# Optimization experiments

Hardware: AMD Instinct MI355X
Metric: run time of the kernel (lower is better)

Reference implementation:

```python
import jax, jax.numpy as jnp
import numpy as np

N_QUBITS = 24          # must be divisible by 3
DIM = 2 ** N_QUBITS    # 16777216 amplitudes
N_GROUPS = N_QUBITS // 3  # 8 disjoint 3-qubit gate applications


def setup_inputs() -> dict:
    key = jax.random.key(0)
    k1, k2, k3 = jax.random.split(key, 3)
    feature = jax.random.normal(k1, (DIM,), dtype=jnp.float32)
    # Build a random 8x8 unitary as expm of an anti-Hermitian generator,
    # mirroring equivar_gate_matrix = expm(generator) in the original.
    m = (jax.random.normal(k2, (8, 8), dtype=jnp.float32)
         + 1j * jax.random.normal(k3, (8, 8), dtype=jnp.float32)).astype(jnp.complex64)
    gen = 0.5 * (m - m.conj().T)
    gate = jax.scipy.linalg.expm(gen)
    return {
        "feature": feature,
        "gate_real": jnp.real(gate).astype(jnp.float32),
        "gate_imag": jnp.imag(gate).astype(jnp.float32),
    }


def _apply_3q_gate(state, gate, axis):
    # state: (8,)*N_GROUPS complex tensor; contract gate (8x8) into `axis`.
    out = jnp.tensordot(gate, state, axes=[[1], [axis]])  # contracted axis -> front
    return jnp.moveaxis(out, 0, axis)


def reference(feature, gate_real, gate_imag):
    # AmplitudeEmbedding: L2-normalize the feature vector into the state.
    norm = jnp.sqrt(jnp.sum(feature * feature))
    state = (feature / norm).astype(jnp.complex64)
    # View the 24 qubits as 8 groups of 3 (each group = one axis of size 8).
    state = state.reshape((8,) * N_GROUPS)
    gate = (gate_real + 1j * gate_imag).astype(jnp.complex64)
    # QubitUnitary(equivar_gate_matrix, wires=(3i, 3i+1, 3i+2)) for each group.
    for g in range(N_GROUPS):
        state = _apply_3q_gate(state, gate, g)
    # qml.probs(): |amplitude|^2 over the full computational basis.
    probs = (jnp.real(state) ** 2 + jnp.imag(state) ** 2).reshape(-1)
    return probs.astype(jnp.float32)
```

## Files before the change

kernel.cpp:

```cpp
#include <hip/hip_runtime.h>


typedef _Float16 f16;
typedef _Float16 f16x4 __attribute__((ext_vector_type(4)));
typedef float f32x4 __attribute__((ext_vector_type(4)));
typedef unsigned int u32;
typedef unsigned short u16;

__device__ __forceinline__ u32 SW1(u32 a) { return a ^ (((a >> 8) & 0xFu) << 3); }
__device__ __forceinline__ u32 SW2(u32 a) { return a ^ (((a >> 7) & 0x7u) << 4); }

__device__ __forceinline__ u32 PK(float x, float y) {
  return __builtin_bit_cast(u32, __builtin_amdgcn_cvt_pkrtz(x, y));
}

__device__ __forceinline__ f16x4 build_A(const float* __restrict__ gr,
                                         const float* __restrict__ gi, int l) {
  const int row = l & 15, kg = l >> 4;
  const int pg = row & 7, rpl = row >> 3, kpl = kg >> 1;
  f16x4 a;
#pragma unroll
  for (int e = 0; e < 4; ++e) {
    const int j = (kg & 1) * 4 + e;
    const float grv = gr[pg * 8 + j], giv = gi[pg * 8 + j];
    const float v = rpl == 0 ? (kpl == 0 ? grv : -giv) : (kpl == 0 ? giv : grv);
    a[e] = (f16)v;
  }
  return a;
}

__device__ __forceinline__ void p1_stage(char* lb, f16x4 A, int w, int l) {
  const int kg = l >> 4, c = l & 15, c3 = c >> 3, p = kg >> 1;
  const u32 rb = (u32)(w * 512 + c * 32 + kg * 8);
  const f32x4 Z = {0.f, 0.f, 0.f, 0.f};
  f32x4 acc[16];
#pragma unroll
  for (int g = 0; g < 4; ++g) {
#pragma unroll
    for (int m = 0; m < 4; ++m) {
      const int j = (g & 1) + m * 2 + (g >> 1) * 8;
      const uint2 bw = *(const uint2*)(lb + SW1(rb + (u32)j * 8192u));
      acc[g * 4 + m] = __builtin_amdgcn_mfma_f32_16x16x16f16(
          A, __builtin_bit_cast(f16x4, bw), Z, 0, 0, 0);
    }
  }
  __syncthreads();
  const u32 wl = (u32)(((w >> 2) << 14) + (((w & 3) * 2 + c3) << 11) +
                       ((c & 7) << 8) + ((kg & 1) << 7) + (p << 4));
#pragma unroll
  for (int g = 0; g < 4; ++g) {
#pragma unroll
    for (int rr = 0; rr < 4; ++rr) {
      const u32 d0 = PK(acc[g * 4 + 0][rr], acc[g * 4 + 1][rr]);
      const u32 d1 = PK(acc[g * 4 + 2][rr], acc[g * 4 + 3][rr]);
      const u32 lg = wl + (u32)(((g & 1) << 16) + ((g >> 1) << 3) + (rr << 5));
      *(uint2*)(lb + SW1(lg)) = make_uint2(d0, d1);
    }
  }
  __syncthreads();
}

__global__ __launch_bounds__(1024, 4) void k_pass1(
    const float* __restrict__ f, const float* __restrict__ gr,
    const float* __restrict__ gi, uint4* __restrict__ st,
    float* __restrict__ wsp) {
  __shared__ __align__(16) char lb[131072];
  __shared__ float red[16];
  const int t = threadIdx.x, l = t & 63, w = t >> 6, blk = blockIdx.x;
  const int kg = l >> 4, c = l & 15, c3 = c >> 3, p = kg >> 1;
  const f16x4 A = build_A(gr, gi, l);
  const f32x4 Z = {0.f, 0.f, 0.f, 0.f};

  float s = 0.f;
  {
    const float* fb = f + ((size_t)blk << 15) + (size_t)(kg & 1) * 16384;
    f32x4 acc[16];
#pragma unroll
    for (int g = 0; g < 4; ++g) {
#pragma unroll
      for (int m = 0; m < 4; ++m) {
        const int j = (g & 1) + m * 2 + (g >> 1) * 8;
        const int col = (j >> 1) * 512 + (j & 1) * 256 + (w >> 2) * 64 +
                        (w & 3) * 16 + c;
        f16x4 b = {(f16)0.f, (f16)0.f, (f16)0.f, (f16)0.f};
        if (kg < 2) {
          const float v0 = fb[col];
          const float v1 = fb[col + 4096];
          const float v2 = fb[col + 8192];
          const float v3 = fb[col + 12288];
          s += v0 * v0 + v1 * v1 + v2 * v2 + v3 * v3;
          b[0] = (f16)v0; b[1] = (f16)v1; b[2] = (f16)v2; b[3] = (f16)v3;
        }
        acc[g * 4 + m] = __builtin_amdgcn_mfma_f32_16x16x16f16(A, b, Z, 0, 0, 0);
      }
    }
    const u32 wl = (u32)(((w >> 2) << 14) + (((w & 3) * 2 + c3) << 11) +
                         ((c & 7) << 8) + ((kg & 1) << 7) + (p << 4));
#pragma unroll
    for (int g = 0; g < 4; ++g) {
#pragma unroll
      for (int rr = 0; rr < 4; ++rr) {
        const u32 d0 = PK(acc[g * 4 + 0][rr], acc[g * 4 + 1][rr]);
        const u32 d1 = PK(acc[g * 4 + 2][rr], acc[g * 4 + 3][rr]);
        const u32 lg = wl + (u32)(((g & 1) << 16) + ((g >> 1) << 3) + (rr << 5));
        *(uint2*)(lb + SW1(lg)) = make_uint2(d0, d1);
      }
    }
  }
#pragma unroll
  for (int off = 32; off; off >>= 1) s += __shfl_down(s, off, 64);
  if (l == 0) red[w] = s;
  __syncthreads();
  if (t == 0) {
    float a = 0.f;
#pragma unroll
    for (int i = 0; i < 16; ++i) a += red[i];
    wsp[blk] = a;
  }

  p1_stage(lb, A, w, l);
  p1_stage(lb, A, w, l);
  p1_stage(lb, A, w, l);

  const u32 rb = (u32)(w * 512 + c * 32 + kg * 8);
  const size_t ob = (size_t)blk * 8192;
#pragma unroll
  for (int j = 0; j < 16; ++j) {
    const uint2 bw = *(const uint2*)(lb + SW1(rb + (u32)j * 8192u));
    const f32x4 a = __builtin_amdgcn_mfma_f32_16x16x16f16(
        A, __builtin_bit_cast(f16x4, bw), Z, 0, 0, 0);
    const u32 h01 = PK(a[0], a[1]), h23 = PK(a[2], a[3]);
    const u32 q01 = __shfl_xor(h01, 32, 64), q23 = __shfl_xor(h23, 32, 64);
    if (p == 0) {
      const int A3 = j >> 1, A4 = (j & 1) * 4 + (w >> 2), A5 = (w & 3) * 2 + c3;
      uint4 vv;
      vv.x = (h01 & 0xffffu) | (q01 << 16);
      vv.y = (h01 >> 16) | (q01 & 0xffff0000u);
      vv.z = (h23 & 0xffffu) | (q23 << 16);
      vv.w = (h23 >> 16) | (q23 & 0xffff0000u);
      st[ob + (u32)(((A3 * 64 + A4 * 8 + A5) << 4) + ((c & 7) << 1) + (kg & 1))] = vv;
    }
  }
}

__device__ __forceinline__ void p2_stage(char* lb, f16x4 A, int w, int l) {
  const int kg = l >> 4, c = l & 15, pp = kg >> 1;
  const f32x4 Z = {0.f, 0.f, 0.f, 0.f};
  f32x4 acc[16];
#pragma unroll
  for (int g = 0; g < 4; ++g) {
#pragma unroll
    for (int m = 0; m < 4; ++m) {
      const int j = (g & 1) + m * 2 + (g >> 1) * 8;
      const u32 rb = (u32)(j * 2048 + w * 512 + c * 32 + kg * 8);
      const uint2 bw = *(const uint2*)(lb + SW2(rb));
      acc[g * 4 + m] = __builtin_amdgcn_mfma_f32_16x16x16f16(
          A, __builtin_bit_cast(f16x4, bw), Z, 0, 0, 0);
    }
  }
  __syncthreads();
#pragma unroll
  for (int pe = 0; pe < 2; ++pe) {
#pragma unroll
    for (int rr = 0; rr < 4; ++rr) {
      uint4 vv;
      vv.x = PK(acc[pe * 4 + 0][rr], acc[pe * 4 + 1][rr]);
      vv.y = PK(acc[pe * 4 + 2][rr], acc[pe * 4 + 3][rr]);
      vv.z = PK(acc[(2 + pe) * 4 + 0][rr], acc[(2 + pe) * 4 + 1][rr]);
      vv.w = PK(acc[(2 + pe) * 4 + 2][rr], acc[(2 + pe) * 4 + 3][rr]);
      const u32 wb = (u32)((pe * 4 + w) * 4096 + ((kg & 1) * 4 + rr) * 512 +
                           c * 32 + pp * 16);
      *(uint4*)(lb + SW2(wb)) = vv;
    }
  }
  __syncthreads();
}

__global__ __launch_bounds__(256, 4) void k_pass2(
    const uint4* gp, const float* __restrict__ gr, const float* __restrict__ gi,
    const float* __restrict__ wsp, float* out) {
  __shared__ __align__(16) char lb[32768];
  __shared__ float red[4];
  const int t = threadIdx.x, l = t & 63, w = t >> 6;
  const int kg = l >> 4, c = l & 15, pp = kg >> 1;
  const int b9 = blockIdx.x >> 2, q = blockIdx.x & 3;
  const f16x4 A = build_A(gr, gi, l);
  const f32x4 Z = {0.f, 0.f, 0.f, 0.f};

  float sp_ = wsp[t] + wsp[t + 256];
#pragma unroll
  for (int off = 32; off; off >>= 1) sp_ += __shfl_down(sp_, off, 64);
  if (l == 0) red[w] = sp_;

  {
    const int z = t >> 2, u = t & 3;
    const int A1 = z & 7, A0 = z >> 3;
#pragma unroll
    for (int a2g = 0; a2g < 2; ++a2g) {
      uint4 raw[4];
#pragma unroll
      for (int d = 0; d < 4; ++d)
        raw[d] = gp[(size_t)(z * 8 + 4 * a2g + d) * 8192 + (u32)(b9 * 16 + q * 4 + u)];
#pragma unroll
      for (int v = 0; v < 4; ++v) {
        const u32 w0 = v == 0 ? raw[0].x : v == 1 ? raw[0].y : v == 2 ? raw[0].z : raw[0].w;
        const u32 w1 = v == 0 ? raw[1].x : v == 1 ? raw[1].y : v == 2 ? raw[1].z : raw[1].w;
        const u32 w2 = v == 0 ? raw[2].x : v == 1 ? raw[2].y : v == 2 ? raw[2].z : raw[2].w;
        const u32 w3 = v == 0 ? raw[3].x : v == 1 ? raw[3].y : v == 2 ? raw[3].z : raw[3].w;
        const int sp = u * 4 + v;
        const u32 base = (u32)(A1 * 4096 + A0 * 512 + sp * 32 + 8 * a2g);
        *(uint2*)(lb + SW2(base)) =
            make_uint2((w0 & 0xffffu) | (w1 << 16), (w2 & 0xffffu) | (w3 << 16));
        *(uint2*)(lb + SW2(base + 16u)) =
            make_uint2((w0 >> 16) | (w1 & 0xffff0000u), (w2 >> 16) | (w3 & 0xffff0000u));
      }
    }
  }
  __syncthreads();
  const float inv = 1.0f / (red[0] + red[1] + red[2] + red[3]);

  p2_stage(lb, A, w, l);
  p2_stage(lb, A, w, l);

#pragma unroll
  for (int j = 0; j < 16; ++j) {
    const u32 rb = (u32)(j * 2048 + w * 512 + c * 32 + kg * 8);
    const uint2 bw = *(const uint2*)(lb + SW2(rb));
    const f32x4 a = __builtin_amdgcn_mfma_f32_16x16x16f16(
        A, __builtin_bit_cast(f16x4, bw), Z, 0, 0, 0);
    const int A2 = j >> 1, A1 = (j & 1) * 4 + w;
    const size_t gb = ((size_t)A1 << 18) + ((size_t)A2 << 15) +
                      (u32)(b9 * 64 + q * 16 + c);
#pragma unroll
    for (int rr = 0; rr < 4; ++rr) {
      float qv = a[rr] * a[rr];
      qv += __shfl_xor(qv, 32, 64);
      if ((rr >> 1) == pp) {
        const size_t A0 = (size_t)((kg & 1) * 4 + rr);
        out[gb + (A0 << 21)] = qv * inv;
      }
    }
  }
}

extern "C" void kernel_launch(void* const* d_in, const int* in_sizes, int n_in,
                              void* d_out, int out_size, void* d_ws,
                              size_t ws_size, hipStream_t stream) {
  (void)in_sizes; (void)n_in; (void)out_size; (void)ws_size;
  const float* f = (const float*)d_in[0];
  const float* gr = (const float*)d_in[1];
  const float* gi = (const float*)d_in[2];
  float* wsp = (float*)d_ws;

  k_pass1<<<dim3(512), dim3(1024), 0, stream>>>(f, gr, gi, (uint4*)d_out, wsp);
  k_pass2<<<dim3(2048), dim3(256), 0, stream>>>((const uint4*)d_out, gr, gi,
                                                wsp, (float*)d_out);
}
```

Measured before the change: 77.75 us.

## Restructure gate passes with warp-private stages, tile looping and vectorized loads

Pass 1 now processes two tiles per block, using 256 blocks instead of 512. The next tile's input is prefetched with float4 loads into registers, and the input is staged through LDS instead of being fed straight into the MFMA. Later contraction stages are remapped so each wavefront reads and writes only its own LDS region, which lets them replace block-wide __syncthreads with an lgkmcnt wait and sched barrier. Pass 2 gets the same warp-private remap for its later stages and a new swizzle. The changes aim to remove block barriers and improve load coalescing, but they make the index mappings more intricate and add an extra LDS staging step.

Measured after the change: 100.2 us. 28.9% more time.

```diff
diff --git a/kernel.cpp b/kernel.cpp
--- a/kernel.cpp
+++ b/kernel.cpp
@@ -5,14 +5,26 @@
 typedef _Float16 f16x4 __attribute__((ext_vector_type(4)));
 typedef float f32x4 __attribute__((ext_vector_type(4)));
 typedef unsigned int u32;
-typedef unsigned short u16;
 
 __device__ __forceinline__ u32 SW1(u32 a) { return a ^ (((a >> 8) & 0xFu) << 3); }
-__device__ __forceinline__ u32 SW2(u32 a) { return a ^ (((a >> 7) & 0x7u) << 4); }
+__device__ __forceinline__ u32 SW2(u32 a) { return a ^ (((a >> 7) & 0xFu) << 3); }
 
 __device__ __forceinline__ u32 PK(float x, float y) {
   return __builtin_bit_cast(u32, __builtin_amdgcn_cvt_pkrtz(x, y));
 }
+
+#define FENCE_LDS()                                     \
+  do {                                                  \
+    asm volatile("s_waitcnt lgkmcnt(0)" ::: "memory");  \
+    __builtin_amdgcn_sched_barrier(0);                  \
+  } while (0)
+
+#define BARRIER_RAW()                                   \
+  do {                                                  \
+    asm volatile("s_waitcnt lgkmcnt(0)" ::: "memory");  \
+    __builtin_amdgcn_sched_barrier(0);                  \
+    __builtin_amdgcn_s_barrier();                       \
+  } while (0)
 
 __device__ __forceinline__ f16x4 build_A(const float* __restrict__ gr,
                                          const float* __restrict__ gi, int l) {
@@ -29,7 +41,13 @@
   return a;
 }
 
-__device__ __forceinline__ void p1_stage(char* lb, f16x4 A, int w, int l) {
+__device__ __forceinline__ f32x4 MF(f16x4 A, uint2 bw, f32x4 C) {
+  return __builtin_amdgcn_mfma_f32_16x16x16f16(A, __builtin_bit_cast(f16x4, bw),
+                                               C, 0, 0, 0);
+}
+
+template <int MODE>
+__device__ __forceinline__ void p1_bw(char* lb, f16x4 A, int w, int l) {
   const int kg = l >> 4, c = l & 15, c3 = c >> 3, p = kg >> 1;
   const u32 rb = (u32)(w * 512 + c * 32 + kg * 8);
   const f32x4 Z = {0.f, 0.f, 0.f, 0.f};
@@ -40,24 +58,121 @@
     for (int m = 0; m < 4; ++m) {
       const int j = (g & 1) + m * 2 + (g >> 1) * 8;
       const uint2 bw = *(const uint2*)(lb + SW1(rb + (u32)j * 8192u));
-      acc[g * 4 + m] = __builtin_amdgcn_mfma_f32_16x16x16f16(
-          A, __builtin_bit_cast(f16x4, bw), Z, 0, 0, 0);
+      acc[g * 4 + m] = MF(A, bw, Z);
     }
   }
   __syncthreads();
-  const u32 wl = (u32)(((w >> 2) << 14) + (((w & 3) * 2 + c3) << 11) +
-                       ((c & 7) << 8) + ((kg & 1) << 7) + (p << 4));
 #pragma unroll
   for (int g = 0; g < 4; ++g) {
 #pragma unroll
     for (int rr = 0; rr < 4; ++rr) {
       const u32 d0 = PK(acc[g * 4 + 0][rr], acc[g * 4 + 1][rr]);
       const u32 d1 = PK(acc[g * 4 + 2][rr], acc[g * 4 + 3][rr]);
-      const u32 lg = wl + (u32)(((g & 1) << 16) + ((g >> 1) << 3) + (rr << 5));
+      u32 lg;
+      if constexpr (MODE == 0) {
+        lg = (u32)(((w >> 2) << 14) + (((w & 3) * 2 + c3) << 11) +
+                   ((c & 7) << 8) + ((kg & 1) << 7) + (p << 4) +
+                   ((g & 1) << 16) + ((g >> 1) << 3) + (rr << 5));
+      } else {
+        lg = (u32)(((c & 7) << 14) + ((kg & 1) << 13) + (rr << 11) +
+                   ((((g & 1) << 2) + (w >> 2)) << 8) +
+                   ((((w & 3) << 1) + c3) << 5) + (p << 4) + ((g >> 1) << 3));
+      }
       *(uint2*)(lb + SW1(lg)) = make_uint2(d0, d1);
     }
   }
   __syncthreads();
+}
+
+__device__ __forceinline__ void p1_priv(char* lb, f16x4 A, int w, int l) {
+  const int kg = l >> 4, c = l & 15, c3 = c >> 3, p = kg >> 1;
+  const f32x4 Z = {0.f, 0.f, 0.f, 0.f};
+  f32x4 acc[16];
+#pragma unroll
+  for (int g = 0; g < 4; ++g) {
+#pragma unroll
+    for (int m = 0; m < 4; ++m) {
+      const u32 rb = (u32)(((4 * w + g) << 11) + (((c3 << 2) + m) << 8) +
+                           ((c & 7) << 5) + (kg << 3));
+      const uint2 bw = *(const uint2*)(lb + SW1(rb));
+      acc[g * 4 + m] = MF(A, bw, Z);
+    }
+  }
+  FENCE_LDS();
+#pragma unroll
+  for (int g = 0; g < 4; ++g) {
+#pragma unroll
+    for (int rr = 0; rr < 4; ++rr) {
+      const u32 d0 = PK(acc[g * 4 + 0][rr], acc[g * 4 + 1][rr]);
+      const u32 d1 = PK(acc[g * 4 + 2][rr], acc[g * 4 + 3][rr]);
+      const u32 lg = (u32)(((4 * w + g) << 11) + ((c & 7) << 8) +
+                           ((((kg & 1) << 2) + rr) << 5) + (p << 4) + (c3 << 3));
+      *(uint2*)(lb + SW1(lg)) = make_uint2(d0, d1);
+    }
+  }
+  FENCE_LDS();
+}
+
+__device__ __forceinline__ void p1_last(char* lb, f16x4 A, int w, int l,
+                                        uint4* __restrict__ st, int tile) {
+  const int kg = l >> 4, c = l & 15, c3 = c >> 3, p = kg >> 1, kg0 = kg & 1;
+  const f32x4 Z = {0.f, 0.f, 0.f, 0.f};
+  const size_t ob = (size_t)tile * 8192;
+#pragma unroll
+  for (int g = 0; g < 4; ++g) {
+#pragma unroll
+    for (int m = 0; m < 4; ++m) {
+      const u32 rb = (u32)(((4 * w + g) << 11) + (((c3 << 2) + m) << 8) +
+                           ((c & 7) << 5) + (kg << 3));
+      const uint2 bw = *(const uint2*)(lb + SW1(rb));
+      const f32x4 a = MF(A, bw, Z);
+      const u32 h01 = PK(a[0], a[1]), h23 = PK(a[2], a[3]);
+      const u32 q01 = __shfl_xor(h01, 32, 64), q23 = __shfl_xor(h23, 32, 64);
+      if (p == 0) {
+        uint4 vv;
+        vv.x = (h01 & 0xffffu) | (q01 << 16);
+        vv.y = (h01 >> 16) | (q01 & 0xffff0000u);
+        vv.z = (h23 & 0xffffu) | (q23 << 16);
+        vv.w = (h23 >> 16) | (q23 & 0xffff0000u);
+        const int combo = 4 * w + g;
+        const int A5v = c3 * 4 + m, A6v = c & 7;
+        st[ob + (u32)(combo * 128 + A5v * 16 + A6v * 2 + kg0)] = vv;
+      }
+    }
+  }
+}
+
+__device__ __forceinline__ float p1_fill(char* lb, const float* __restrict__ f,
+                                         int tile, int t, const float4* pre) {
+  const float4* fin = (const float4*)f + (size_t)tile * 8192;
+  float4 hi4[4];
+#pragma unroll
+  for (int d = 0; d < 4; ++d) hi4[d] = fin[(4 + d) * 1024 + t];
+  const u32 fl = (u32)(((t >> 7) << 14) | (((t >> 4) & 7) << 11) |
+                       (((t >> 1) & 7) << 8) | ((t & 1) << 7));
+  float s = 0.f;
+#pragma unroll
+  for (int g2 = 0; g2 < 2; ++g2) {
+    const float4 v0 = g2 ? hi4[0] : pre[0];
+    const float4 v1 = g2 ? hi4[1] : pre[1];
+    const float4 v2 = g2 ? hi4[2] : pre[2];
+    const float4 v3 = g2 ? hi4[3] : pre[3];
+    s += v0.x * v0.x + v0.y * v0.y + v0.z * v0.z + v0.w * v0.w;
+    s += v1.x * v1.x + v1.y * v1.y + v1.z * v1.z + v1.w * v1.w;
+    s += v2.x * v2.x + v2.y * v2.y + v2.z * v2.z + v2.w * v2.w;
+    s += v3.x * v3.x + v3.y * v3.y + v3.z * v3.z + v3.w * v3.w;
+#pragma unroll
+    for (int q = 0; q < 4; ++q) {
+      const float a0 = q == 0 ? v0.x : q == 1 ? v0.y : q == 2 ? v0.z : v0.w;
+      const float a1 = q == 0 ? v1.x : q == 1 ? v1.y : q == 2 ? v1.z : v1.w;
+      const float a2 = q == 0 ? v2.x : q == 1 ? v2.y : q == 2 ? v2.z : v2.w;
+      const float a3 = q == 0 ? v3.x : q == 1 ? v3.y : q == 2 ? v3.z : v3.w;
+      const u32 lg = fl + (u32)((q << 5) + (g2 << 3));
+      *(uint2*)(lb + SW1(lg)) = make_uint2(PK(a0, a1), PK(a2, a3));
+      *(uint2*)(lb + SW1(lg + 16u)) = make_uint2(0u, 0u);
+    }
+  }
+  return s;
 }
 
 __global__ __launch_bounds__(1024, 4) void k_pass1(
@@ -67,148 +182,78 @@
   __shared__ __align__(16) char lb[131072];
   __shared__ float red[16];
   const int t = threadIdx.x, l = t & 63, w = t >> 6, blk = blockIdx.x;
-  const int kg = l >> 4, c = l & 15, c3 = c >> 3, p = kg >> 1;
   const f16x4 A = build_A(gr, gi, l);
-  const f32x4 Z = {0.f, 0.f, 0.f, 0.f};
-
-  float s = 0.f;
-  {
-    const float* fb = f + ((size_t)blk << 15) + (size_t)(kg & 1) * 16384;
-    f32x4 acc[16];
-#pragma unroll
-    for (int g = 0; g < 4; ++g) {
-#pragma unroll
-      for (int m = 0; m < 4; ++m) {
-        const int j = (g & 1) + m * 2 + (g >> 1) * 8;
-        const int col = (j >> 1) * 512 + (j & 1) * 256 + (w >> 2) * 64 +
-                        (w & 3) * 16 + c;
-        f16x4 b = {(f16)0.f, (f16)0.f, (f16)0.f, (f16)0.f};
-        if (kg < 2) {
-          const float v0 = fb[col];
-          const float v1 = fb[col + 4096];
-          const float v2 = fb[col + 8192];
-          const float v3 = fb[col + 12288];
-          s += v0 * v0 + v1 * v1 + v2 * v2 + v3 * v3;
-          b[0] = (f16)v0; b[1] = (f16)v1; b[2] = (f16)v2; b[3] = (f16)v3;
-        }
-        acc[g * 4 + m] = __builtin_amdgcn_mfma_f32_16x16x16f16(A, b, Z, 0, 0, 0);
-      }
-    }
-    const u32 wl = (u32)(((w >> 2) << 14) + (((w & 3) * 2 + c3) << 11) +
-                         ((c & 7) << 8) + ((kg & 1) << 7) + (p << 4));
-#pragma unroll
-    for (int g = 0; g < 4; ++g) {
-#pragma unroll
-      for (int rr = 0; rr < 4; ++rr) {
-        const u32 d0 = PK(acc[g * 4 + 0][rr], acc[g * 4 + 1][rr]);
-        const u32 d1 = PK(acc[g * 4 + 2][rr], acc[g * 4 + 3][rr]);
-        const u32 lg = wl + (u32)(((g & 1) << 16) + ((g >> 1) << 3) + (rr << 5));
-        *(uint2*)(lb + SW1(lg)) = make_uint2(d0, d1);
-      }
-    }
-  }
-#pragma unroll
-  for (int off = 32; off; off >>= 1) s += __shfl_down(s, off, 64);
-  if (l == 0) red[w] = s;
-  __syncthreads();
-  if (t == 0) {
-    float a = 0.f;
-#pragma unroll
-    for (int i = 0; i < 16; ++i) a += red[i];
-    wsp[blk] = a;
-  }
-
-  p1_stage(lb, A, w, l);
-  p1_stage(lb, A, w, l);
-  p1_stage(lb, A, w, l);
-
-  const u32 rb = (u32)(w * 512 + c * 32 + kg * 8);
-  const size_t ob = (size_t)blk * 8192;
-#pragma unroll
-  for (int j = 0; j < 16; ++j) {
-    const uint2 bw = *(const uint2*)(lb + SW1(rb + (u32)j * 8192u));
-    const f32x4 a = __builtin_amdgcn_mfma_f32_16x16x16f16(
-        A, __builtin_bit_cast(f16x4, bw), Z, 0, 0, 0);
-    const u32 h01 = PK(a[0], a[1]), h23 = PK(a[2], a[3]);
-    const u32 q01 = __shfl_xor(h01, 32, 64), q23 = __shfl_xor(h23, 32, 64);
-    if (p == 0) {
-      const int A3 = j >> 1, A4 = (j & 1) * 4 + (w >> 2), A5 = (w & 3) * 2 + c3;
-      uint4 vv;
-      vv.x = (h01 & 0xffffu) | (q01 << 16);
-      vv.y = (h01 >> 16) | (q01 & 0xffff0000u);
-      vv.z = (h23 & 0xffffu) | (q23 << 16);
-      vv.w = (h23 >> 16) | (q23 & 0xffff0000u);
-      st[ob + (u32)(((A3 * 64 + A4 * 8 + A5) << 4) + ((c & 7) << 1) + (kg & 1))] = vv;
-    }
-  }
-}
-
-__device__ __forceinline__ void p2_stage(char* lb, f16x4 A, int w, int l) {
-  const int kg = l >> 4, c = l & 15, pp = kg >> 1;
-  const f32x4 Z = {0.f, 0.f, 0.f, 0.f};
-  f32x4 acc[16];
-#pragma unroll
-  for (int g = 0; g < 4; ++g) {
-#pragma unroll
-    for (int m = 0; m < 4; ++m) {
-      const int j = (g & 1) + m * 2 + (g >> 1) * 8;
-      const u32 rb = (u32)(j * 2048 + w * 512 + c * 32 + kg * 8);
-      const uint2 bw = *(const uint2*)(lb + SW2(rb));
-      acc[g * 4 + m] = __builtin_amdgcn_mfma_f32_16x16x16f16(
-          A, __builtin_bit_cast(f16x4, bw), Z, 0, 0, 0);
-    }
-  }
-  __syncthreads();
-#pragma unroll
-  for (int pe = 0; pe < 2; ++pe) {
-#pragma unroll
-    for (int rr = 0; rr < 4; ++rr) {
-      uint4 vv;
-      vv.x = PK(acc[pe * 4 + 0][rr], acc[pe * 4 + 1][rr]);
-      vv.y = PK(acc[pe * 4 + 2][rr], acc[pe * 4 + 3][rr]);
-      vv.z = PK(acc[(2 + pe) * 4 + 0][rr], acc[(2 + pe) * 4 + 1][rr]);
-      vv.w = PK(acc[(2 + pe) * 4 + 2][rr], acc[(2 + pe) * 4 + 3][rr]);
-      const u32 wb = (u32)((pe * 4 + w) * 4096 + ((kg & 1) * 4 + rr) * 512 +
-                           c * 32 + pp * 16);
-      *(uint4*)(lb + SW2(wb)) = vv;
-    }
-  }
-  __syncthreads();
+  float nrm = 0.f;
+  float4 pre[4];
+  {
+    const float4* fin = (const float4*)f + (size_t)(blk * 2) * 8192;
+#pragma unroll
+    for (int d = 0; d < 4; ++d) pre[d] = fin[d * 1024 + t];
+  }
+#pragma unroll
+  for (int tt = 0; tt < 2; ++tt) {
+    const int tile = blk * 2 + tt;
+    float s = p1_fill(lb, f, tile, t, pre);
+#pragma unroll
+    for (int off = 32; off; off >>= 1) s += __shfl_down(s, off, 64);
+    if (l == 0) red[w] = s;
+    __syncthreads();
+    if (t == 0) {
+      float a = 0.f;
+#pragma unroll
+      for (int i = 0; i < 16; ++i) a += red[i];
+      nrm += a;
+    }
+    p1_bw<0>(lb, A, w, l);
+    p1_bw<1>(lb, A, w, l);
+    if (tt == 0) {
+      const float4* fin = (const float4*)f + (size_t)(blk * 2 + 1) * 8192;
+#pragma unroll
+      for (int d = 0; d < 4; ++d) pre[d] = fin[d * 1024 + t];
+    }
+    p1_priv(lb, A, w, l);
+    p1_priv(lb, A, w, l);
+    p1_last(lb, A, w, l, st, tile);
+    if (tt == 0) BARRIER_RAW();
+  }
+  if (t == 0) wsp[blk] = nrm;
 }
 
 __global__ __launch_bounds__(256, 4) void k_pass2(
-    const uint4* gp, const float* __restrict__ gr, const float* __restrict__ gi,
-    const float* __restrict__ wsp, float* out) {
+    const uint4* __restrict__ gp, const float* __restrict__ gr,
+    const float* __restrict__ gi, const float* __restrict__ wsp,
+    float* __restrict__ out) {
   __shared__ __align__(16) char lb[32768];
   __shared__ float red[4];
   const int t = threadIdx.x, l = t & 63, w = t >> 6;
-  const int kg = l >> 4, c = l & 15, pp = kg >> 1;
+  const int kg = l >> 4, c = l & 15, kg0 = kg & 1, kg1 = kg >> 1;
   const int b9 = blockIdx.x >> 2, q = blockIdx.x & 3;
   const f16x4 A = build_A(gr, gi, l);
   const f32x4 Z = {0.f, 0.f, 0.f, 0.f};
 
-  float sp_ = wsp[t] + wsp[t + 256];
+  float sp_ = wsp[t];
 #pragma unroll
   for (int off = 32; off; off >>= 1) sp_ += __shfl_down(sp_, off, 64);
   if (l == 0) red[w] = sp_;
 
   {
     const int z = t >> 2, u = t & 3;
-    const int A1 = z & 7, A0 = z >> 3;
+    const int A0v = z >> 3, A1v = z & 7;
 #pragma unroll
     for (int a2g = 0; a2g < 2; ++a2g) {
       uint4 raw[4];
 #pragma unroll
       for (int d = 0; d < 4; ++d)
-        raw[d] = gp[(size_t)(z * 8 + 4 * a2g + d) * 8192 + (u32)(b9 * 16 + q * 4 + u)];
+        raw[d] = gp[(size_t)(z * 8 + a2g * 4 + d) * 8192 +
+                    (u32)(b9 * 16 + q * 4 + u)];
 #pragma unroll
       for (int v = 0; v < 4; ++v) {
         const u32 w0 = v == 0 ? raw[0].x : v == 1 ? raw[0].y : v == 2 ? raw[0].z : raw[0].w;
         const u32 w1 = v == 0 ? raw[1].x : v == 1 ? raw[1].y : v == 2 ? raw[1].z : raw[1].w;
         const u32 w2 = v == 0 ? raw[2].x : v == 1 ? raw[2].y : v == 2 ? raw[2].z : raw[2].w;
         const u32 w3 = v == 0 ? raw[3].x : v == 1 ? raw[3].y : v == 2 ? raw[3].z : raw[3].w;
-        const int sp = u * 4 + v;
-        const u32 base = (u32)(A1 * 4096 + A0 * 512 + sp * 32 + 8 * a2g);
+        const int spv = u * 4 + v;
+        const u32 base = (u32)((A1v << 12) + (A0v << 9) + (spv << 5) + (a2g << 3));
         *(uint2*)(lb + SW2(base)) =
             make_uint2((w0 & 0xffffu) | (w1 << 16), (w2 & 0xffffu) | (w3 << 16));
         *(uint2*)(lb + SW2(base + 16u)) =
@@ -219,25 +264,95 @@
   __syncthreads();
   const float inv = 1.0f / (red[0] + red[1] + red[2] + red[3]);
 
-  p2_stage(lb, A, w, l);
-  p2_stage(lb, A, w, l);
-
-#pragma unroll
-  for (int j = 0; j < 16; ++j) {
-    const u32 rb = (u32)(j * 2048 + w * 512 + c * 32 + kg * 8);
-    const uint2 bw = *(const uint2*)(lb + SW2(rb));
-    const f32x4 a = __builtin_amdgcn_mfma_f32_16x16x16f16(
-        A, __builtin_bit_cast(f16x4, bw), Z, 0, 0, 0);
-    const int A2 = j >> 1, A1 = (j & 1) * 4 + w;
-    const size_t gb = ((size_t)A1 << 18) + ((size_t)A2 << 15) +
-                      (u32)(b9 * 64 + q * 16 + c);
-#pragma unroll
-    for (int rr = 0; rr < 4; ++rr) {
-      float qv = a[rr] * a[rr];
-      qv += __shfl_xor(qv, 32, 64);
-      if ((rr >> 1) == pp) {
-        const size_t A0 = (size_t)((kg & 1) * 4 + rr);
-        out[gb + (A0 << 21)] = qv * inv;
+  {
+    f32x4 acc[16];
+#pragma unroll
+    for (int g = 0; g < 4; ++g) {
+#pragma unroll
+      for (int m = 0; m < 4; ++m) {
+        const int j = (g & 1) + m * 2 + (g >> 1) * 8;
+        const u32 rb = (u32)(((j >> 1) << 12) + ((((j & 1) << 2) + w) << 9) +
+                             (c << 5) + (kg << 3));
+        const uint2 bw = *(const uint2*)(lb + SW2(rb));
+        acc[g * 4 + m] = MF(A, bw, Z);
+      }
+    }
+    __syncthreads();
+#pragma unroll
+    for (int g = 0; g < 4; ++g) {
+#pragma unroll
+      for (int rr = 0; rr < 4; ++rr) {
+        const u32 d0 = PK(acc[g * 4 + 0][rr], acc[g * 4 + 1][rr]);
+        const u32 d1 = PK(acc[g * 4 + 2][rr], acc[g * 4 + 3][rr]);
+        const u32 lg = (u32)((((kg0 << 2) + rr) << 12) + (c << 8) +
+                             ((((g & 1) << 2) + w) << 5) + (kg1 << 4) +
+                             ((g >> 1) << 3));
+        *(uint2*)(lb + SW2(lg)) = make_uint2(d0, d1);
+      }
+    }
+    __syncthreads();
+  }
+
+  const int c0 = c & 1, ch = c >> 1;
+
+  {
+    f32x4 acc[16];
+#pragma unroll
+    for (int G = 0; G < 4; ++G) {
+#pragma unroll
+      for (int m = 0; m < 4; ++m) {
+        const u32 rb = (u32)(((2 * w + (G >> 1)) << 12) +
+                             ((((G & 1) << 3) + ch) << 8) +
+                             (((c0 << 2) + m) << 5) + (kg << 3));
+        const uint2 bw = *(const uint2*)(lb + SW2(rb));
+        acc[G * 4 + m] = MF(A, bw, Z);
+      }
+    }
+    FENCE_LDS();
+#pragma unroll
+    for (int G = 0; G < 4; ++G) {
+#pragma unroll
+      for (int rr = 0; rr < 4; ++rr) {
+        const u32 d0 = PK(acc[G * 4 + 0][rr], acc[G * 4 + 1][rr]);
+        const u32 d1 = PK(acc[G * 4 + 2][rr], acc[G * 4 + 3][rr]);
+        const u32 lg = (u32)(((2 * w + (G >> 1)) << 12) +
+                             ((((G & 1) << 3) + ch) << 8) +
+                             (((kg0 << 2) + rr) << 5) + (kg1 << 4) + (c0 << 3));
+        *(uint2*)(lb + SW2(lg)) = make_uint2(d0, d1);
+      }
+    }
+    FENCE_LDS();
+  }
+
+  {
+    const u32 nbase = (u32)(b9 * 64 + q * 16);
+#pragma unroll
+    for (int G = 0; G < 4; ++G) {
+#pragma unroll
+      for (int m = 0; m < 4; ++m) {
+        const u32 rb = (u32)(((2 * w + (G >> 1)) << 12) +
+                             ((((G & 1) << 3) + ch) << 8) +
+                             (((c0 << 2) + m) << 5) + (kg << 3));
+        const uint2 bw = *(const uint2*)(lb + SW2(rb));
+        const f32x4 a = MF(A, bw, Z);
+        float qv0 = a[0] * a[0]; qv0 += __shfl_xor(qv0, 32, 64);
+        float qv1 = a[1] * a[1]; qv1 += __shfl_xor(qv1, 32, 64);
+        float qv2 = a[2] * a[2]; qv2 += __shfl_xor(qv2, 32, 64);
+        float qv3 = a[3] * a[3]; qv3 += __shfl_xor(qv3, 32, 64);
+        const int A1v = c0 * 4 + m, A2v = 2 * w + (G >> 1);
+        const int spv = (G & 1) * 8 + ch;
+        const size_t base = ((size_t)A1v << 18) + ((size_t)A2v << 15) +
+                            (size_t)(nbase + spv);
+        {
+          const float val = (kg1 ? qv2 : qv0) * inv;
+          const size_t A0v = (size_t)(kg0 * 4 + kg1 * 2);
+          out[base + (A0v << 21)] = val;
+        }
+        {
+          const float val = (kg1 ? qv3 : qv1) * inv;
+          const size_t A0v = (size_t)(kg0 * 4 + kg1 * 2 + 1);
+          out[base + (A0v << 21)] = val;
+        }
       }
     }
   }
@@ -252,7 +367,7 @@
   const float* gi = (const float*)d_in[2];
   float* wsp = (float*)d_ws;
 
-  k_pass1<<<dim3(512), dim3(1024), 0, stream>>>(f, gr, gi, (uint4*)d_out, wsp);
+  k_pass1<<<dim3(256), dim3(1024), 0, stream>>>(f, gr, gi, (uint4*)d_out, wsp);
   k_pass2<<<dim3(2048), dim3(256), 0, stream>>>((const uint4*)d_out, gr, gi,
                                                 wsp, (float*)d_out);
 }
```
